# Kernel optimization log

Hardware: AMD Instinct MI355X
Metric: run time of the kernel (lower is better)

Reference implementation:

```python
import jax, jax.numpy as jnp
import numpy as np

N_NODES = 65536
IN_CH = 512
HIDDEN = 256          # hidden_channels[0] == encoder_hidden
OUT_CH = 8
NUM_GRAPHS = 32
MAX_LEN = 4096        # static pad bound (>= max per-graph length)
BN_EPS = 1e-5


def _make_batch_ids():
    # deterministic ragged per-graph lengths summing exactly to N_NODES
    rng = np.random.RandomState(0)
    d = rng.randint(-512, 512, size=NUM_GRAPHS)
    d[-1] -= d.sum()
    lengths = N_NODES // NUM_GRAPHS + d          # each in ~[1536, 2560] <= MAX_LEN
    return jnp.asarray(np.repeat(np.arange(NUM_GRAPHS), lengths), dtype=jnp.int32)


def setup_inputs() -> dict:
    key = jax.random.key(0)
    ks = jax.random.split(key, 12)
    f32 = jnp.float32
    inp = {
        'x_res': jax.random.normal(ks[0], (N_NODES, IN_CH), dtype=f32),
        'batch': _make_batch_ids(),
        # BatchNorm1d affine params
        'bn_gamma': jnp.ones((IN_CH,), f32),
        'bn_beta': jnp.zeros((IN_CH,), f32),
        # input2transformer: Linear(C,2H) GELU Linear(2H,H) GELU Linear(H,H)
        'W1': jax.random.normal(ks[1], (IN_CH, 2 * HIDDEN), f32) * (1.0 / np.sqrt(IN_CH)),
        'b1': jnp.zeros((2 * HIDDEN,), f32),
        'W2': jax.random.normal(ks[2], (2 * HIDDEN, HIDDEN), f32) * (1.0 / np.sqrt(2 * HIDDEN)),
        'b2': jnp.zeros((HIDDEN,), f32),
        'W3': jax.random.normal(ks[3], (HIDDEN, HIDDEN), f32) * (1.0 / np.sqrt(HIDDEN)),
        'b3': jnp.zeros((HIDDEN,), f32),
        # out_angles: Linear(encoder_hidden, out_ch) GELU DynamicTanh Tanh
        'Wo': jax.random.normal(ks[4], (HIDDEN, OUT_CH), f32) * (1.0 / np.sqrt(HIDDEN)),
        'bo': jnp.zeros((OUT_CH,), f32),
        'dyt_alpha': jnp.asarray(0.5, f32),
        'dyt_w': jnp.ones((OUT_CH,), f32),
        'dyt_b': jnp.zeros((OUT_CH,), f32),
    }
    return inp


def _forward(x_res, batch, bn_gamma, bn_beta, W1, b1, W2, b2, W3, b3,
             Wo, bo, dyt_alpha, dyt_w, dyt_b):
    # BatchNorm1d (training-mode batch stats, biased var), dropout is identity (eval)
    mu = jnp.mean(x_res, axis=0)
    var = jnp.mean((x_res - mu) ** 2, axis=0)
    x = (x_res - mu) * jax.lax.rsqrt(var + BN_EPS) * bn_gamma + bn_beta
    # input2transformer MLP (torch GELU default = exact erf)
    gelu = lambda t: jax.nn.gelu(t, approximate=False)
    x = gelu(x @ W1 + b1)
    x = gelu(x @ W2 + b2)
    x = x @ W3 + b3                                   # [N, HIDDEN]
    # ragged -> padded: scatter each node into (graph, position-in-graph)
    counts = jax.ops.segment_sum(jnp.ones_like(batch, dtype=jnp.int32), batch,
                                 num_segments=NUM_GRAPHS)
    offsets = jnp.concatenate([jnp.zeros((1,), jnp.int32),
                               jnp.cumsum(counts)[:-1].astype(jnp.int32)])
    pos = jnp.arange(N_NODES, dtype=jnp.int32) - offsets[batch]
    x_pad = jnp.zeros((NUM_GRAPHS, MAX_LEN, HIDDEN), x.dtype).at[batch, pos].set(x)
    z = jnp.transpose(x_pad, (1, 0, 2))               # [MAX_LEN, NUM_GRAPHS, HIDDEN] (stack dim=1)
    # out_angles head: Linear -> GELU -> DynamicTanh -> Tanh
    a = gelu(z @ Wo + bo)
    a = dyt_w * jnp.tanh(dyt_alpha * a) + dyt_b       # DynamicTanh (channels_last)
    return jnp.tanh(a)                                # [MAX_LEN, NUM_GRAPHS, OUT_CH]


def reference(x_res, batch, bn_gamma, bn_beta, W1, b1, W2, b2, W3, b3,
              Wo, bo, dyt_alpha, dyt_w, dyt_b):
    return _forward(x_res, batch, bn_gamma, bn_beta, W1, b1, W2, b2, W3, b3,
                    Wo, bo, dyt_alpha, dyt_w, dyt_b)
```

## Files before the change

### kernel.cpp

```cpp
#include <hip/hip_runtime.h>
#include <hip/hip_bf16.h>

#define N_NODES 65536
#define IN_CH 512
#define HIDDEN 256
#define OUT_CH 8
#define NUM_GRAPHS 32
#define MAX_LEN 4096
#define BN_EPS 1e-5f
#define BN_BLOCKS 2048

using short8  = __attribute__((ext_vector_type(8))) short;
using floatx4 = __attribute__((ext_vector_type(4))) float;
typedef unsigned int u32;
typedef unsigned short u16;

__device__ inline u16 f2b(float f) {
    u32 u = __float_as_uint(f);
    u += 0x7FFFu + ((u >> 16) & 1u);
    return (u16)(u >> 16);
}
__device__ inline float gelu_f(float x) {
    float z = x + 0.044715f * x * x * x;
    float e = __builtin_exp2f(-2.3022078f * z);
    return x * __builtin_amdgcn_rcpf(1.0f + e);
}
__device__ inline float tanh_f(float y) {
    y = fminf(fmaxf(y, -20.0f), 20.0f);
    float t = __builtin_exp2f(2.885390082f * y);
    return (t - 1.0f) * __builtin_amdgcn_rcpf(t + 1.0f);
}
__device__ inline void load_lds16(const void* g, void* l) {
    __builtin_amdgcn_global_load_lds(
        (const __attribute__((address_space(1))) u32*)g,
        (__attribute__((address_space(3))) u32*)l, 16, 0, 0);
}

__global__ __launch_bounds__(256) void statscast_k(const float* __restrict__ x,
                                                   u16* __restrict__ xb,
                                                   float4* __restrict__ partials) {
    __shared__ float4 sS[128];
    __shared__ float4 sQ[128];
    int tid = threadIdx.x;
    int half = tid >> 7;
    int c = tid & 127;
    const float4* x4 = (const float4*)x;
    uint2* xb2 = (uint2*)xb;
    float4 s = make_float4(0.f, 0.f, 0.f, 0.f);
    float4 q = make_float4(0.f, 0.f, 0.f, 0.f);
    int row0 = blockIdx.x * 32;
#pragma unroll
    for (int r = half; r < 32; r += 2) {
        size_t off = (size_t)(row0 + r) * 128 + c;
        float4 v = x4[off];
        s.x += v.x; s.y += v.y; s.z += v.z; s.w += v.w;
        q.x += v.x * v.x; q.y += v.y * v.y; q.z += v.z * v.z; q.w += v.w * v.w;
        uint2 o;
        o.x = (u32)f2b(v.x) | ((u32)f2b(v.y) << 16);
        o.y = (u32)f2b(v.z) | ((u32)f2b(v.w) << 16);
        xb2[off] = o;
    }
    if (half == 1) { sS[c] = s; sQ[c] = q; }
    __syncthreads();
    if (half == 0) {
        float4 s2 = sS[c], q2 = sQ[c];
        s.x += s2.x; s.y += s2.y; s.z += s2.z; s.w += s2.w;
        q.x += q2.x; q.y += q2.y; q.z += q2.z; q.w += q2.w;
        partials[(size_t)blockIdx.x * 256 + c * 2]     = make_float4(s.x, q.x, s.y, q.y);
        partials[(size_t)blockIdx.x * 256 + c * 2 + 1] = make_float4(s.z, q.z, s.w, q.w);
    }
}

__global__ __launch_bounds__(256) void bn_reduce_k(const float4* __restrict__ partials,
                                                   const float* __restrict__ gamma,
                                                   const float* __restrict__ beta,
                                                   float* __restrict__ scale,
                                                   float* __restrict__ shift) {
    __shared__ float4 sd[256];
    int tid = threadIdx.x;
    int g = blockIdx.x;
    float4 a = make_float4(0.f, 0.f, 0.f, 0.f);
    for (int r = tid; r < BN_BLOCKS; r += 256) {
        float4 v = partials[(size_t)r * 256 + g];
        a.x += v.x; a.y += v.y; a.z += v.z; a.w += v.w;
    }
    sd[tid] = a;
    __syncthreads();
    for (int st = 128; st > 0; st >>= 1) {
        if (tid < st) {
            float4 b = sd[tid + st];
            float4 m = sd[tid];
            m.x += b.x; m.y += b.y; m.z += b.z; m.w += b.w;
            sd[tid] = m;
        }
        __syncthreads();
    }
    if (tid == 0) {
        float4 t = sd[0];
        int c0 = g * 2, c1 = g * 2 + 1;
        const float inv = 1.0f / N_NODES;
        float mu0 = t.x * inv, var0 = t.y * inv - mu0 * mu0;
        float mu1 = t.z * inv, var1 = t.w * inv - mu1 * mu1;
        float sc0 = gamma[c0] * rsqrtf(var0 + BN_EPS);
        float sc1 = gamma[c1] * rsqrtf(var1 + BN_EPS);
        scale[c0] = sc0; shift[c0] = beta[c0] - mu0 * sc0;
        scale[c1] = sc1; shift[c1] = beta[c1] - mu1 * sc1;
    }
}

__global__ __launch_bounds__(256) void prep_k(const float* __restrict__ W1,
                                              const float* __restrict__ W2,
                                              const float* __restrict__ W3,
                                              const float* __restrict__ b1,
                                              const float* __restrict__ scale,
                                              const float* __restrict__ shift,
                                              u16* __restrict__ W1T,
                                              u16* __restrict__ W2T,
                                              u16* __restrict__ W3T,
                                              float* __restrict__ b1f,
                                              const int* __restrict__ batch,
                                              int* __restrict__ offsets) {
    int bid = blockIdx.x;
    int tid = threadIdx.x;
    if (bid < 1792) {
        int idx = bid * 256 + tid;
        if (idx < 262144) {
            int k = idx >> 9, m = idx & 511;
            W1T[(size_t)m * 512 + k] = f2b(scale[k] * W1[idx]);
        } else if (idx < 262144 + 131072) {
            int i = idx - 262144;
            int k = i >> 8, m = i & 255;
            W2T[(size_t)m * 512 + k] = f2b(W2[i]);
        } else {
            int i = idx - 393216;
            int k = i >> 8, m = i & 255;
            W3T[(size_t)m * 256 + k] = f2b(W3[i]);
        }
        if (bid == 0 && tid < NUM_GRAPHS + 1) {
            int gph = tid;
            int lo = 0, hi = N_NODES;
            while (lo < hi) {
                int mid = (lo + hi) >> 1;
                if (batch[mid] < gph) lo = mid + 1; else hi = mid;
            }
            offsets[gph] = lo;
        }
    } else {
        int m = (bid - 1792) * 256 + tid;
        float acc = b1[m];
#pragma unroll 16
        for (int k = 0; k < 512; ++k) acc += shift[k] * W1[k * 512 + m];
        b1f[m] = acc;
    }
}

template <int DO_GELU, int NXB>
__global__ __launch_bounds__(512) void gemm_bt_k(const u16* __restrict__ A,
                                                 const u16* __restrict__ BT,
                                                 const float* __restrict__ bias,
                                                 u16* __restrict__ C,
                                                 int K, int M) {
    __shared__ __align__(16) u16 As[256 * 64];
    __shared__ __align__(16) u16 Bs[128 * 64];
    int tid = threadIdx.x;
    int lane = tid & 63;
    int bid = blockIdx.x;
    int xcd = bid & 7;
    int slot = bid >> 3;
    int rloc = slot / NXB;
    int colb = slot - rloc * NXB;
    int row0 = (xcd * 32 + rloc) * 256;
    int col0 = colb * 128;
    int wave = tid >> 6;
    int wr = (wave >> 1) * 64;
    int wc = (wave & 1) * 64;
    int l15 = lane & 15;
    int q = lane >> 4;

    floatx4 acc[4][4] = {};

    const int nkt = K >> 6;
    for (int kt = 0; kt < nkt; ++kt) {
        int k0 = kt << 6;
#pragma unroll
        for (int s = 0; s < 4; ++s) {
            int li = s * 512 + tid;
            int r = li >> 3;
            int g = li & 7;
            int gs = g ^ (r & 7);
            load_lds16(&A[(size_t)(row0 + r) * K + k0 + gs * 8], &As[li * 8]);
        }
#pragma unroll
        for (int s = 0; s < 2; ++s) {
            int li = s * 512 + tid;
            int r = li >> 3;
            int g = li & 7;
            int gs = g ^ (r & 7);
            load_lds16(&BT[(size_t)(col0 + r) * K + k0 + gs * 8], &Bs[li * 8]);
        }
        __syncthreads();
#pragma unroll
        for (int ks = 0; ks < 2; ++ks) {
            int gidx = ks * 4 + q;
            short8 af[4], bg[4];
#pragma unroll
            for (int i = 0; i < 4; ++i) {
                int row = wr + i * 16 + l15;
                af[i] = *(const short8*)&As[row * 64 + (gidx ^ (row & 7)) * 8];
            }
#pragma unroll
            for (int j = 0; j < 4; ++j) {
                int row = wc + j * 16 + l15;
                bg[j] = *(const short8*)&Bs[row * 64 + (gidx ^ (row & 7)) * 8];
            }
#pragma unroll
            for (int i = 0; i < 4; ++i)
#pragma unroll
                for (int j = 0; j < 4; ++j)
                    acc[i][j] = __builtin_amdgcn_mfma_f32_16x16x32_bf16(bg[j], af[i], acc[i][j], 0, 0, 0);
        }
        __syncthreads();
    }
#pragma unroll
    for (int i = 0; i < 4; ++i) {
        size_t rbase = (size_t)(row0 + wr + i * 16 + l15) * M;
#pragma unroll
        for (int j = 0; j < 4; ++j) {
            int c = col0 + wc + j * 16 + q * 4;
            float4 b4 = *(const float4*)&bias[c];
            float v0 = acc[i][j][0] + b4.x;
            float v1 = acc[i][j][1] + b4.y;
            float v2 = acc[i][j][2] + b4.z;
            float v3 = acc[i][j][3] + b4.w;
            if (DO_GELU) { v0 = gelu_f(v0); v1 = gelu_f(v1); v2 = gelu_f(v2); v3 = gelu_f(v3); }
            uint2 pk;
            pk.x = (u32)f2b(v0) | ((u32)f2b(v1) << 16);
            pk.y = (u32)f2b(v2) | ((u32)f2b(v3) << 16);
            *(uint2*)&C[rbase + c] = pk;
        }
    }
}

#define FENCE asm volatile("" ::: "memory")

__global__ __launch_bounds__(512, 2) void gemm23_k(const u16* __restrict__ A,
                                                   const u16* __restrict__ B2T,
                                                   const float* __restrict__ b2v,
                                                   const u16* __restrict__ W3T,
                                                   const float* __restrict__ b3v,
                                                   u16* __restrict__ C) {
    __shared__ __align__(16) u16 lds[65536];
    int tid = threadIdx.x;
    int lane = tid & 63;
    int bid = blockIdx.x;
    int xcd = bid & 7;
    int slot = bid >> 3;
    int row0 = (xcd * 32 + slot) * 256;
    int wave = tid >> 6;
    int wr = (wave >> 2) * 128;
    int wc = (wave & 3) * 64;
    int l15 = lane & 15;
    int q = lane >> 4;

    floatx4 acc[8][4] = {};

    const u16* pA[4];
    const u16* pB[4];
    int ldst[4];
#pragma unroll
    for (int s = 0; s < 4; ++s) {
        int li = s * 512 + tid;
        int r = li >> 3;
        int g = li & 7;
        int gs = g ^ (r & 7);
        pA[s] = A + (size_t)(row0 + r) * 512 + gs * 8;
        pB[s] = B2T + (size_t)r * 512 + gs * 8;
        ldst[s] = li * 8;
    }

#define LDA2(BASE, GIDX)                                                             \
    _Pragma("unroll")                                                                \
    for (int i = 0; i < 4; ++i) {                                                    \
        int row = (BASE) + i * 16 + l15;                                             \
        af[i] = *(const short8*)&lds[curA + row * 64 + (((GIDX) ^ (row & 7)) << 3)]; \
    }
#define LDB2(BASE, GIDX)                                                             \
    _Pragma("unroll")                                                                \
    for (int j = 0; j < 4; ++j) {                                                    \
        int row = (BASE) + j * 16 + l15;                                             \
        bg[j] = *(const short8*)&lds[curB + row * 64 + (((GIDX) ^ (row & 7)) << 3)]; \
    }
#define MFMA16(IB)                                                                   \
    __builtin_amdgcn_s_setprio(1);                                                   \
    _Pragma("unroll")                                                                \
    for (int i = 0; i < 4; ++i)                                                      \
        _Pragma("unroll")                                                            \
        for (int j = 0; j < 4; ++j)                                                  \
            acc[(IB) + i][j] = __builtin_amdgcn_mfma_f32_16x16x32_bf16(              \
                bg[j], af[i], acc[(IB) + i][j], 0, 0, 0);                            \
    __builtin_amdgcn_s_setprio(0)

#pragma unroll
    for (int s = 0; s < 4; ++s) load_lds16(pA[s], &lds[ldst[s]]);
#pragma unroll
    for (int s = 0; s < 4; ++s) load_lds16(pB[s], &lds[32768 + ldst[s]]);

    const int nt = 8;
    for (int t = 0; t < nt; ++t) {
        const int cur = t & 1;
        const int nx = cur ^ 1;
        const bool last = (t + 1 == nt);
        const int kn = (t + 1) << 6;
        const int curA = cur * 16384, curB = 32768 + cur * 16384;
        const int nxA = nx * 16384,  nxB = 32768 + nx * 16384;
        short8 af[4], bg[4];

        if (!last) {
            load_lds16(pA[0] + kn, &lds[nxA + ldst[0]]);
            load_lds16(pA[1] + kn, &lds[nxA + ldst[1]]);
        }
        if (last) asm volatile("s_waitcnt vmcnt(0)" ::: "memory");
        else      asm volatile("s_waitcnt vmcnt(2)" ::: "memory");
        __builtin_amdgcn_s_barrier();
        FENCE;
        LDA2(wr, q);
        LDB2(wc, q);
        MFMA16(0);
        FENCE;
        __builtin_amdgcn_s_barrier();
        LDA2(wr + 64, q);
        if (!last) {
            load_lds16(pA[2] + kn, &lds[nxA + ldst[2]]);
            load_lds16(pA[3] + kn, &lds[nxA + ldst[3]]);
        }
        FENCE;
        __builtin_amdgcn_s_barrier();
        FENCE;
        MFMA16(4);
        FENCE;
        __builtin_amdgcn_s_barrier();
        LDA2(wr, 4 + q);
        LDB2(wc, 4 + q);
        if (!last) {
            load_lds16(pB[0] + kn, &lds[nxB + ldst[0]]);
            load_lds16(pB[1] + kn, &lds[nxB + ldst[1]]);
        }
        FENCE;
        __builtin_amdgcn_s_barrier();
        FENCE;
        MFMA16(0);
        FENCE;
        __builtin_amdgcn_s_barrier();
        LDA2(wr + 64, 4 + q);
        if (!last) {
            load_lds16(pB[2] + kn, &lds[nxB + ldst[2]]);
            load_lds16(pB[3] + kn, &lds[nxB + ldst[3]]);
        }
        FENCE;
        __builtin_amdgcn_s_barrier();
        FENCE;
        MFMA16(4);
        FENCE;
        __builtin_amdgcn_s_barrier();
        FENCE;
    }
    __syncthreads();

#pragma unroll
    for (int i = 0; i < 8; ++i) {
        int row = wr + i * 16 + l15;
#pragma unroll
        for (int j = 0; j < 4; ++j) {
            int c = wc + j * 16 + q * 4;
            float4 b4 = *(const float4*)&b2v[c];
            float v0 = gelu_f(acc[i][j][0] + b4.x);
            float v1 = gelu_f(acc[i][j][1] + b4.y);
            float v2 = gelu_f(acc[i][j][2] + b4.z);
            float v3 = gelu_f(acc[i][j][3] + b4.w);
            uint2 pk;
            pk.x = (u32)f2b(v0) | ((u32)f2b(v1) << 16);
            pk.y = (u32)f2b(v2) | ((u32)f2b(v3) << 16);
            int gr = c >> 3;
            int addr = row * 256 + ((gr ^ (row & 7)) << 3) + (q & 1) * 4;
            *(uint2*)&lds[addr] = pk;
        }
    }
    __syncthreads();

#pragma unroll
    for (int i = 0; i < 8; ++i)
#pragma unroll
        for (int j = 0; j < 4; ++j)
            acc[i][j] = (floatx4){0.f, 0.f, 0.f, 0.f};

    for (int ks = 0; ks < 8; ++ks) {
        int gidx = ks * 4 + q;
        short8 af[8], bg[4];
#pragma unroll
        for (int j = 0; j < 4; ++j) {
            int colr = wc + j * 16 + l15;
            bg[j] = *(const short8*)&W3T[(size_t)colr * 256 + gidx * 8];
        }
#pragma unroll
        for (int i = 0; i < 8; ++i) {
            int row = wr + i * 16 + l15;
            af[i] = *(const short8*)&lds[row * 256 + ((gidx ^ (row & 7)) << 3)];
        }
        __builtin_amdgcn_s_setprio(1);
#pragma unroll
        for (int i = 0; i < 8; ++i)
#pragma unroll
            for (int j = 0; j < 4; ++j)
                acc[i][j] = __builtin_amdgcn_mfma_f32_16x16x32_bf16(bg[j], af[i], acc[i][j], 0, 0, 0);
        __builtin_amdgcn_s_setprio(0);
    }

#pragma unroll
    for (int i = 0; i < 8; ++i) {
        size_t rbase = (size_t)(row0 + wr + i * 16 + l15) * 256;
#pragma unroll
        for (int j = 0; j < 4; ++j) {
            int c = wc + j * 16 + q * 4;
            float4 b4 = *(const float4*)&b3v[c];
            float v0 = acc[i][j][0] + b4.x;
            float v1 = acc[i][j][1] + b4.y;
            float v2 = acc[i][j][2] + b4.z;
            float v3 = acc[i][j][3] + b4.w;
            uint2 pk;
            pk.x = (u32)f2b(v0) | ((u32)f2b(v1) << 16);
            pk.y = (u32)f2b(v2) | ((u32)f2b(v3) << 16);
            *(uint2*)&C[rbase + c] = pk;
        }
    }
#undef LDA2
#undef LDB2
#undef MFMA16
}

__global__ __launch_bounds__(256) void head_k(const u16* __restrict__ h3,
                                              const float* __restrict__ Wo,
                                              const float* __restrict__ bo,
                                              const int* __restrict__ offsets,
                                              const float* __restrict__ alpha_p,
                                              const float* __restrict__ dyt_w,
                                              const float* __restrict__ dyt_b,
                                              float* __restrict__ out) {
    __shared__ float sWo[HIDDEN * OUT_CH];
    __shared__ int soff[NUM_GRAPHS + 1];
    int tid = threadIdx.x;
#pragma unroll
    for (int i = 0; i < 8; ++i) sWo[i * 256 + tid] = Wo[i * 256 + tid];
    if (tid < NUM_GRAPHS + 1) soff[tid] = offsets[tid];
    __syncthreads();
    int idx = blockIdx.x * 256 + tid;
    int g = idx & 31;
    int p = idx >> 5;
    int n = soff[g] + p;
    bool valid = n < soff[g + 1];
    float acc[8];
#pragma unroll
    for (int c = 0; c < 8; ++c) acc[c] = bo[c];
    if (valid) {
        const uint4* hr = (const uint4*)(h3 + (size_t)n * HIDDEN);
#pragma unroll 4
        for (int kk = 0; kk < 32; ++kk) {
            uint4 v = hr[kk];
            u32 u[4] = {v.x, v.y, v.z, v.w};
#pragma unroll
            for (int pp = 0; pp < 4; ++pp) {
                float h0 = __uint_as_float(u[pp] << 16);
                float h1 = __uint_as_float(u[pp] & 0xFFFF0000u);
                const float* w0 = &sWo[(kk * 8 + pp * 2) * 8];
                const float* w1 = w0 + 8;
#pragma unroll
                for (int c = 0; c < 8; ++c) acc[c] += h0 * w0[c];
#pragma unroll
                for (int c = 0; c < 8; ++c) acc[c] += h1 * w1[c];
            }
        }
    }
    float alpha = alpha_p[0];
    float res[8];
#pragma unroll
    for (int c = 0; c < 8; ++c) {
        float a = gelu_f(acc[c]);
        a = dyt_w[c] * tanh_f(alpha * a) + dyt_b[c];
        res[c] = tanh_f(a);
    }
    float4* o = (float4*)(out + (size_t)idx * OUT_CH);
    o[0] = make_float4(res[0], res[1], res[2], res[3]);
    o[1] = make_float4(res[4], res[5], res[6], res[7]);
}

extern "C" void kernel_launch(void* const* d_in, const int* in_sizes, int n_in,
                              void* d_out, int out_size, void* d_ws, size_t ws_size,
                              hipStream_t stream) {
    (void)in_sizes; (void)n_in; (void)out_size; (void)ws_size;
    const float* x_res = (const float*)d_in[0];
    const int*   batch = (const int*)d_in[1];
    const float* gamma = (const float*)d_in[2];
    const float* beta  = (const float*)d_in[3];
    const float* W1    = (const float*)d_in[4];
    const float* b1    = (const float*)d_in[5];
    const float* W2    = (const float*)d_in[6];
    const float* b2    = (const float*)d_in[7];
    const float* W3    = (const float*)d_in[8];
    const float* b3    = (const float*)d_in[9];
    const float* Wo    = (const float*)d_in[10];
    const float* bo    = (const float*)d_in[11];
    const float* alpha = (const float*)d_in[12];
    const float* dyt_w = (const float*)d_in[13];
    const float* dyt_b = (const float*)d_in[14];
    float* out = (float*)d_out;

    char* ws = (char*)d_ws;
    float* scale = (float*)(ws + 0);
    float* shift = (float*)(ws + 2048);
    float* b1f   = (float*)(ws + 4096);
    int*   offs  = (int*)(ws + 8192);
    u16* W1T = (u16*)(ws + 16384);
    u16* W2T = (u16*)(ws + 16384 + 524288);
    u16* W3T = (u16*)(ws + 16384 + 524288 + 262144);
    const size_t MB = 1024 * 1024;
    u16* xb = (u16*)(ws + 2 * MB);
    u16* h1 = (u16*)(ws + 66 * MB);
    u16* h3 = (u16*)(ws + 2 * MB);
    float4* partials = (float4*)(ws + 66 * MB);

    statscast_k<<<BN_BLOCKS, 256, 0, stream>>>(x_res, xb, partials);
    bn_reduce_k<<<256, 256, 0, stream>>>(partials, gamma, beta, scale, shift);
    prep_k<<<1794, 256, 0, stream>>>(W1, W2, W3, b1, scale, shift,
                                     W1T, W2T, W3T, b1f, batch, offs);
    gemm_bt_k<1, 4><<<1024, 512, 0, stream>>>(xb, W1T, b1f, h1, 512, 512);
    gemm23_k<<<256, 512, 0, stream>>>(h1, W2T, b2, W3T, b3, h3);
    head_k<<<512, 256, 0, stream>>>(h3, Wo, bo, offs, alpha, dyt_w, dyt_b, out);
}
```

Measured before the change: 374.3 us.

## Fuse output head into GEMM2/3 kernel and fill padding rows in prep

The Wo head (Linear, GELU, DynamicTanh, Tanh) now runs in the epilogue of the fused GEMM2/GEMM3 kernel. The bf16 h3 tile is staged through swizzled LDS, and each pair of threads computes four output channels for one node, scattering the result into the padded [MAX_LEN, graph] layout. Padding positions, which only depend on the bias, are written by extra blocks added to the prep kernel. This drops the h3 global write and read round-trip and one kernel launch. In exchange the GEMM kernel gains extra syncs, LDS traffic, a per-row binary search over offsets, and scattered stores.

```diff
diff --git a/kernel.cpp b/kernel.cpp
--- a/kernel.cpp
+++ b/kernel.cpp
@@ -119,7 +119,13 @@
                                               u16* __restrict__ W3T,
                                               float* __restrict__ b1f,
                                               const int* __restrict__ batch,
-                                              int* __restrict__ offsets) {
+                                              int* __restrict__ offsets,
+                                              const float* __restrict__ bo,
+                                              const float* __restrict__ alpha_p,
+                                              const float* __restrict__ dyt_w,
+                                              const float* __restrict__ dyt_b,
+                                              float* __restrict__ out) {
+    __shared__ int sof2[NUM_GRAPHS + 1];
     int bid = blockIdx.x;
     int tid = threadIdx.x;
     if (bid < 1792) {
@@ -145,12 +151,39 @@
             }
             offsets[gph] = lo;
         }
-    } else {
+    } else if (bid < 1794) {
         int m = (bid - 1792) * 256 + tid;
         float acc = b1[m];
 #pragma unroll 16
         for (int k = 0; k < 512; ++k) acc += shift[k] * W1[k * 512 + m];
         b1f[m] = acc;
+    } else {
+        if (tid < NUM_GRAPHS + 1) {
+            int target = tid;
+            int lo = 0, hi = N_NODES;
+            while (lo < hi) {
+                int mid = (lo + hi) >> 1;
+                if (batch[mid] < target) lo = mid + 1; else hi = mid;
+            }
+            sof2[tid] = lo;
+        }
+        __syncthreads();
+        int idx = (bid - 1794) * 256 + tid;
+        int g = idx & 31;
+        int p = idx >> 5;
+        if (p >= sof2[g + 1] - sof2[g]) {
+            float alpha = alpha_p[0];
+            float rv[8];
+#pragma unroll
+            for (int c = 0; c < 8; ++c) {
+                float a = gelu_f(bo[c]);
+                a = dyt_w[c] * tanh_f(alpha * a) + dyt_b[c];
+                rv[c] = tanh_f(a);
+            }
+            float4* o = (float4*)(out + (size_t)idx * OUT_CH);
+            o[0] = make_float4(rv[0], rv[1], rv[2], rv[3]);
+            o[1] = make_float4(rv[4], rv[5], rv[6], rv[7]);
+        }
     }
 }
 
@@ -243,13 +276,21 @@
 
 #define FENCE asm volatile("" ::: "memory")
 
-__global__ __launch_bounds__(512, 2) void gemm23_k(const u16* __restrict__ A,
-                                                   const u16* __restrict__ B2T,
-                                                   const float* __restrict__ b2v,
-                                                   const u16* __restrict__ W3T,
-                                                   const float* __restrict__ b3v,
-                                                   u16* __restrict__ C) {
+__global__ __launch_bounds__(512, 2) void gemm23h_k(const u16* __restrict__ A,
+                                                    const u16* __restrict__ B2T,
+                                                    const float* __restrict__ b2v,
+                                                    const u16* __restrict__ W3T,
+                                                    const float* __restrict__ b3v,
+                                                    const float* __restrict__ Wo,
+                                                    const float* __restrict__ bo,
+                                                    const int* __restrict__ offsets,
+                                                    const float* __restrict__ alpha_p,
+                                                    const float* __restrict__ dyt_w,
+                                                    const float* __restrict__ dyt_b,
+                                                    float* __restrict__ out) {
     __shared__ __align__(16) u16 lds[65536];
+    __shared__ float sWo[HIDDEN * OUT_CH];
+    __shared__ int soff[NUM_GRAPHS + 1];
     int tid = threadIdx.x;
     int lane = tid & 63;
     int bid = blockIdx.x;
@@ -261,6 +302,9 @@
     int wc = (wave & 3) * 64;
     int l15 = lane & 15;
     int q = lane >> 4;
+
+    ((float4*)sWo)[tid] = ((const float4*)Wo)[tid];
+    if (tid < NUM_GRAPHS + 1) soff[tid] = offsets[tid];
 
     floatx4 acc[8][4] = {};
 
@@ -414,10 +458,11 @@
                 acc[i][j] = __builtin_amdgcn_mfma_f32_16x16x32_bf16(bg[j], af[i], acc[i][j], 0, 0, 0);
         __builtin_amdgcn_s_setprio(0);
     }
+    __syncthreads();
 
 #pragma unroll
     for (int i = 0; i < 8; ++i) {
-        size_t rbase = (size_t)(row0 + wr + i * 16 + l15) * 256;
+        int row = wr + i * 16 + l15;
 #pragma unroll
         for (int j = 0; j < 4; ++j) {
             int c = wc + j * 16 + q * 4;
@@ -429,67 +474,53 @@
             uint2 pk;
             pk.x = (u32)f2b(v0) | ((u32)f2b(v1) << 16);
             pk.y = (u32)f2b(v2) | ((u32)f2b(v3) << 16);
-            *(uint2*)&C[rbase + c] = pk;
-        }
+            int gr = c >> 3;
+            int addr = row * 256 + ((gr ^ (row & 31)) << 3) + (q & 1) * 4;
+            *(uint2*)&lds[addr] = pk;
+        }
+    }
+    __syncthreads();
+
+    {
+        int r = tid >> 1;
+        int chalf = (tid & 1) * 4;
+        int n = row0 + r;
+        int lo = 0, hi = NUM_GRAPHS;
+        while (hi - lo > 1) {
+            int mid = (lo + hi) >> 1;
+            if (soff[mid] <= n) lo = mid; else hi = mid;
+        }
+        int g = lo;
+        int p = n - soff[g];
+        float4 a4 = *(const float4*)&bo[chalf];
+#pragma unroll 4
+        for (int kk = 0; kk < 32; ++kk) {
+            short8 h = *(const short8*)&lds[r * 256 + ((kk ^ (r & 31)) << 3)];
+#pragma unroll
+            for (int e = 0; e < 8; ++e) {
+                float hv = __uint_as_float((u32)(u16)h[e] << 16);
+                const float* w = &sWo[(kk * 8 + e) * 8 + chalf];
+                a4.x += hv * w[0];
+                a4.y += hv * w[1];
+                a4.z += hv * w[2];
+                a4.w += hv * w[3];
+            }
+        }
+        float alpha = alpha_p[0];
+        float av[4] = {a4.x, a4.y, a4.z, a4.w};
+        float rv[4];
+#pragma unroll
+        for (int c = 0; c < 4; ++c) {
+            float a = gelu_f(av[c]);
+            a = dyt_w[chalf + c] * tanh_f(alpha * a) + dyt_b[chalf + c];
+            rv[c] = tanh_f(a);
+        }
+        *(float4*)&out[((size_t)(p * NUM_GRAPHS + g)) * 8 + chalf] =
+            make_float4(rv[0], rv[1], rv[2], rv[3]);
     }
 #undef LDA2
 #undef LDB2
 #undef MFMA16
-}
-
-__global__ __launch_bounds__(256) void head_k(const u16* __restrict__ h3,
-                                              const float* __restrict__ Wo,
-                                              const float* __restrict__ bo,
-                                              const int* __restrict__ offsets,
-                                              const float* __restrict__ alpha_p,
-                                              const float* __restrict__ dyt_w,
-                                              const float* __restrict__ dyt_b,
-                                              float* __restrict__ out) {
-    __shared__ float sWo[HIDDEN * OUT_CH];
-    __shared__ int soff[NUM_GRAPHS + 1];
-    int tid = threadIdx.x;
-#pragma unroll
-    for (int i = 0; i < 8; ++i) sWo[i * 256 + tid] = Wo[i * 256 + tid];
-    if (tid < NUM_GRAPHS + 1) soff[tid] = offsets[tid];
-    __syncthreads();
-    int idx = blockIdx.x * 256 + tid;
-    int g = idx & 31;
-    int p = idx >> 5;
-    int n = soff[g] + p;
-    bool valid = n < soff[g + 1];
-    float acc[8];
-#pragma unroll
-    for (int c = 0; c < 8; ++c) acc[c] = bo[c];
-    if (valid) {
-        const uint4* hr = (const uint4*)(h3 + (size_t)n * HIDDEN);
-#pragma unroll 4
-        for (int kk = 0; kk < 32; ++kk) {
-            uint4 v = hr[kk];
-            u32 u[4] = {v.x, v.y, v.z, v.w};
-#pragma unroll
-            for (int pp = 0; pp < 4; ++pp) {
-                float h0 = __uint_as_float(u[pp] << 16);
-                float h1 = __uint_as_float(u[pp] & 0xFFFF0000u);
-                const float* w0 = &sWo[(kk * 8 + pp * 2) * 8];
-                const float* w1 = w0 + 8;
-#pragma unroll
-                for (int c = 0; c < 8; ++c) acc[c] += h0 * w0[c];
-#pragma unroll
-                for (int c = 0; c < 8; ++c) acc[c] += h1 * w1[c];
-            }
-        }
-    }
-    float alpha = alpha_p[0];
-    float res[8];
-#pragma unroll
-    for (int c = 0; c < 8; ++c) {
-        float a = gelu_f(acc[c]);
-        a = dyt_w[c] * tanh_f(alpha * a) + dyt_b[c];
-        res[c] = tanh_f(a);
-    }
-    float4* o = (float4*)(out + (size_t)idx * OUT_CH);
-    o[0] = make_float4(res[0], res[1], res[2], res[3]);
-    o[1] = make_float4(res[4], res[5], res[6], res[7]);
 }
 
 extern "C" void kernel_launch(void* const* d_in, const int* in_sizes, int n_in,
@@ -524,14 +555,14 @@
     const size_t MB = 1024 * 1024;
     u16* xb = (u16*)(ws + 2 * MB);
     u16* h1 = (u16*)(ws + 66 * MB);
-    u16* h3 = (u16*)(ws + 2 * MB);
     float4* partials = (float4*)(ws + 66 * MB);
 
     statscast_k<<<BN_BLOCKS, 256, 0, stream>>>(x_res, xb, partials);
     bn_reduce_k<<<256, 256, 0, stream>>>(partials, gamma, beta, scale, shift);
-    prep_k<<<1794, 256, 0, stream>>>(W1, W2, W3, b1, scale, shift,
-                                     W1T, W2T, W3T, b1f, batch, offs);
+    prep_k<<<2306, 256, 0, stream>>>(W1, W2, W3, b1, scale, shift,
+                                     W1T, W2T, W3T, b1f, batch, offs,
+                                     bo, alpha, dyt_w, dyt_b, out);
     gemm_bt_k<1, 4><<<1024, 512, 0, stream>>>(xb, W1T, b1f, h1, 512, 512);
-    gemm23_k<<<256, 512, 0, stream>>>(h1, W2T, b2, W3T, b3, h3);
-    head_k<<<512, 256, 0, stream>>>(h3, Wo, bo, offs, alpha, dyt_w, dyt_b, out);
-}
+    gemm23h_k<<<256, 512, 0, stream>>>(h1, W2T, b2, W3T, b3, Wo, bo, offs,
+                                       alpha, dyt_w, dyt_b, out);
+}
```

Measured after the change: 353.2 us. -5.6%, faster.
